# Optimization experiments

Measured on AMD Instinct MI355X. Metric: run time of the kernel, lower is better.

Reference implementation:

```python
import jax, jax.numpy as jnp
import numpy as np

NUM_BINS = 10
HIST_RANGE = 10.0
LN_EPS = 1e-5
NUM_SERVERS = 64
START_IDX = 2 + 2 + NUM_SERVERS  # = 68


def layer_norm(x, g, b):
    mu = jnp.mean(x, axis=-1, keepdims=True)
    var = jnp.mean(jnp.square(x - mu), axis=-1, keepdims=True)
    return (x - mu) * jax.lax.rsqrt(var + LN_EPS) * g + b


def batched_histogram(w):
    # w: [B, S]; replicates np.histogram(w_i, bins=10, range=(0,10)) per row,
    # then normalizes by (sum + 1e-8). Values outside [0,10] are excluded;
    # value == 10 falls in the last bin.
    idx = jnp.clip(jnp.floor(w * (NUM_BINS / HIST_RANGE)).astype(jnp.int32), 0, NUM_BINS - 1)
    mask = ((w >= 0.0) & (w <= HIST_RANGE)).astype(w.dtype)
    oh = jax.nn.one_hot(idx, NUM_BINS, dtype=w.dtype) * mask[..., None]  # [B,S,NB]
    hist = jnp.sum(oh, axis=1)  # [B,NB]
    return hist / (jnp.sum(hist, axis=-1, keepdims=True) + 1e-8)


def setup_inputs() -> dict:
    key = jax.random.key(0)
    ks = jax.random.split(key, 16)
    B, OBS, ACT, H, NB = 65536, 512, 64, 128, NUM_BINS
    COMB = (OBS - NUM_SERVERS) + 128 + 64  # 640

    def lin(k, fin, fout):
        bound = 1.0 / np.sqrt(fin)
        kw, kb = jax.random.split(k)
        return (jax.random.uniform(kw, (fin, fout), jnp.float32, -bound, bound),
                jax.random.uniform(kb, (fout,), jnp.float32, -bound, bound))

    obs = jax.random.uniform(ks[0], (B, OBS), jnp.float32, 0.0, 10.0)
    preference = jax.random.uniform(ks[1], (B, 2), jnp.float32)
    h_w1, h_b1 = lin(ks[2], NB, H)
    h_w2, h_b2 = lin(ks[3], H, H)
    p_w, p_b = lin(ks[4], 2, 64)
    s_w1, s_b1 = lin(ks[5], COMB, 256)
    s_w2, s_b2 = lin(ks[6], 256, 256)
    qd_w, qd_b = lin(ks[7], 256, ACT)
    qe_w, qe_b = lin(ks[8], 256, ACT)
    return {
        'obs': obs, 'preference': preference,
        'h_w1': h_w1, 'h_b1': h_b1,
        'h_ln1_g': jnp.ones((H,)), 'h_ln1_b': jnp.zeros((H,)),
        'h_w2': h_w2, 'h_b2': h_b2,
        'h_ln2_g': jnp.ones((H,)), 'h_ln2_b': jnp.zeros((H,)),
        'p_w': p_w, 'p_b': p_b,
        'p_ln_g': jnp.ones((64,)), 'p_ln_b': jnp.zeros((64,)),
        's_w1': s_w1, 's_b1': s_b1,
        's_ln1_g': jnp.ones((256,)), 's_ln1_b': jnp.zeros((256,)),
        's_w2': s_w2, 's_b2': s_b2,
        's_ln2_g': jnp.ones((256,)), 's_ln2_b': jnp.zeros((256,)),
        'qd_w': qd_w, 'qd_b': qd_b, 'qe_w': qe_w, 'qe_b': qe_b,
    }


def reference(obs, preference,
              h_w1, h_b1, h_ln1_g, h_ln1_b, h_w2, h_b2, h_ln2_g, h_ln2_b,
              p_w, p_b, p_ln_g, p_ln_b,
              s_w1, s_b1, s_ln1_g, s_ln1_b, s_w2, s_b2, s_ln2_g, s_ln2_b,
              qd_w, qd_b, qe_w, qe_b):
    server_workloads = obs[:, START_IDX:START_IDX + NUM_SERVERS]
    obs_wo = jnp.concatenate([obs[:, :START_IDX], obs[:, START_IDX + NUM_SERVERS:]], axis=-1)

    hist = batched_histogram(server_workloads)  # [B, 10]
    h = layer_norm(jax.nn.relu(hist @ h_w1 + h_b1), h_ln1_g, h_ln1_b)
    h = layer_norm(jax.nn.relu(h @ h_w2 + h_b2), h_ln2_g, h_ln2_b)  # [B,128]

    p = layer_norm(jax.nn.relu(preference @ p_w + p_b), p_ln_g, p_ln_b)  # [B,64]

    combined = jnp.concatenate([obs_wo, h, p], axis=-1)  # [B,640]
    s = layer_norm(jax.nn.relu(combined @ s_w1 + s_b1), s_ln1_g, s_ln1_b)
    s = layer_norm(jax.nn.relu(s @ s_w2 + s_b2), s_ln2_g, s_ln2_b)  # [B,256]

    q_delay = s @ qd_w + qd_b   # [B,A]
    q_energy = s @ qe_w + qe_b  # [B,A]
    return jnp.stack([q_delay, q_energy], axis=-1)  # [B,A,2]
```

## Files before the change

kernel.cpp:

```cpp
#include <hip/hip_runtime.h>

typedef __bf16 bf16x8 __attribute__((ext_vector_type(8)));
typedef __bf16 bf16x4 __attribute__((ext_vector_type(4)));
typedef float  f32x4  __attribute__((ext_vector_type(4)));

#define OFF_W1  0
#define OFF_W2  163840
#define OFF_WQ  229376
#define OFF_WH1 262144
#define OFF_WH2 266240
#define WS_ELEMS 282624

__global__ __launch_bounds__(256) void prep_kernel(
    const float* __restrict__ s_w1, const float* __restrict__ s_w2,
    const float* __restrict__ qd_w, const float* __restrict__ qe_w,
    const float* __restrict__ h_w1, const float* __restrict__ h_w2,
    __bf16* __restrict__ wsb)
{
  int idx = blockIdx.x * 256 + threadIdx.x;
  if (idx >= WS_ELEMS) return;
  float val = 0.f;
  if (idx < OFF_W2) {
    int t = idx;
    int j = t & 7, l = (t >> 3) & 63, rest = t >> 9;
    int nt = rest & 15, ks = rest >> 4;
    int k = ks * 32 + (l >> 4) * 8 + j, n = nt * 16 + (l & 15);
    val = s_w1[k * 256 + n];
  } else if (idx < OFF_WQ) {
    int t = idx - OFF_W2;
    int j = t & 7, l = (t >> 3) & 63, rest = t >> 9;
    int nt = rest & 15, ks = rest >> 4;
    int k = ks * 32 + (l >> 4) * 8 + j, n = nt * 16 + (l & 15);
    val = s_w2[k * 256 + n];
  } else if (idx < OFF_WH1) {
    int t = idx - OFF_WQ;
    int j = t & 7, l = (t >> 3) & 63, rest = t >> 9;
    int nt = rest & 7, ks = rest >> 3;
    int k = ks * 32 + (l >> 4) * 8 + j, n = nt * 16 + (l & 15);
    int a = n >> 1;
    val = (n & 1) ? qe_w[k * 64 + a] : qd_w[k * 64 + a];
  } else if (idx < OFF_WH2) {
    int t = idx - OFF_WH1;
    int j = t & 7, l = (t >> 3) & 63, rest = t >> 9;
    int nt = rest & 7;
    int k = (l >> 4) * 8 + j, n = nt * 16 + (l & 15);
    val = (k < 10) ? h_w1[k * 128 + n] : 0.f;
  } else {
    int t = idx - OFF_WH2;
    int j = t & 7, l = (t >> 3) & 63, rest = t >> 9;
    int nt = rest & 7, ks = rest >> 3;
    int k = ks * 32 + (l >> 4) * 8 + j, n = nt * 16 + (l & 15);
    val = h_w2[k * 128 + n];
  }
  wsb[idx] = (__bf16)val;
}

template<int KSTEPS, int NT_TOT, int NTW>
__device__ __forceinline__ void run_gemm(const __bf16* A, int astride,
    const bf16x8* __restrict__ Bsw, int wave, int lane, f32x4 acc[NTW])
{
  const int quad = lane >> 4, ln = lane & 15;
  const int ntb = wave * NTW;
  bf16x8 bcur[NTW];
#pragma unroll
  for (int i = 0; i < NTW; ++i) bcur[i] = Bsw[(ntb + i) * 64 + lane];
#pragma unroll
  for (int ks = 0; ks < KSTEPS; ++ks) {
    bf16x8 bnxt[NTW];
    if (ks + 1 < KSTEPS) {
#pragma unroll
      for (int i = 0; i < NTW; ++i)
        bnxt[i] = Bsw[((ks + 1) * NT_TOT + ntb + i) * 64 + lane];
    }
    bf16x8 a = *(const bf16x8*)(A + ln * astride + ks * 32 + quad * 8);
#pragma unroll
    for (int i = 0; i < NTW; ++i)
      acc[i] = __builtin_amdgcn_mfma_f32_16x16x32_bf16(a, bcur[i], acc[i], 0, 0, 0);
    if (ks + 1 < KSTEPS) {
#pragma unroll
      for (int i = 0; i < NTW; ++i) bcur[i] = bnxt[i];
    }
  }
}

template<int W, int NTW>
__device__ __forceinline__ void epilogue_ln(f32x4 acc[NTW],
    const float* __restrict__ bias, const float* __restrict__ g, const float* __restrict__ bb,
    __bf16* Adst, int dstride, int dstcol0,
    float2* red, int wave, int lane)
{
  const int quad = lane >> 4, ln = lane & 15;
  float x[NTW][4];
#pragma unroll
  for (int i = 0; i < NTW; ++i) {
    int n = (wave * NTW + i) * 16 + ln;
    float b = bias[n];
#pragma unroll
    for (int r = 0; r < 4; ++r)
      x[i][r] = fmaxf(acc[i][r] + b, 0.f);
  }
  float s[4] = {0, 0, 0, 0}, q[4] = {0, 0, 0, 0};
#pragma unroll
  for (int i = 0; i < NTW; ++i)
#pragma unroll
    for (int r = 0; r < 4; ++r) { s[r] += x[i][r]; q[r] += x[i][r] * x[i][r]; }
#pragma unroll
  for (int m2 = 1; m2 < 16; m2 <<= 1)
#pragma unroll
    for (int r = 0; r < 4; ++r) {
      s[r] += __shfl_xor(s[r], m2, 64);
      q[r] += __shfl_xor(q[r], m2, 64);
    }
  if (ln == 0) {
#pragma unroll
    for (int r = 0; r < 4; ++r)
      red[wave * 16 + quad * 4 + r] = make_float2(s[r], q[r]);
  }
  __syncthreads();
#pragma unroll
  for (int r = 0; r < 4; ++r) {
    int m = quad * 4 + r;
    float tot = 0.f, totq = 0.f;
#pragma unroll
    for (int w2 = 0; w2 < 8; ++w2) {
      float2 t = red[w2 * 16 + m];
      tot += t.x; totq += t.y;
    }
    float mu = tot / (float)W;
    float var = totq / (float)W - mu * mu;
    float rs = rsqrtf(var + 1e-5f);
#pragma unroll
    for (int i = 0; i < NTW; ++i) {
      int n = (wave * NTW + i) * 16 + ln;
      float o = (x[i][r] - mu) * rs * g[n] + bb[n];
      Adst[m * dstride + dstcol0 + n] = (__bf16)o;
    }
  }
  __syncthreads();
}

__global__ __launch_bounds__(512, 8) void critic_kernel(
    const float* __restrict__ obs, const float* __restrict__ pref,
    const float* __restrict__ h_b1, const float* __restrict__ h_g1, const float* __restrict__ h_bb1,
    const float* __restrict__ h_b2, const float* __restrict__ h_g2, const float* __restrict__ h_bb2,
    const float* __restrict__ p_w, const float* __restrict__ p_b,
    const float* __restrict__ p_g, const float* __restrict__ p_bb,
    const float* __restrict__ s_b1, const float* __restrict__ s_g1, const float* __restrict__ s_bb1,
    const float* __restrict__ s_b2, const float* __restrict__ s_g2, const float* __restrict__ s_bb2,
    const float* __restrict__ qd_b, const float* __restrict__ qe_b,
    const __bf16* __restrict__ wsb, float* __restrict__ out)
{
  __shared__ __align__(16) __bf16 A_comb[16 * 648];
  __shared__ __align__(16) __bf16 A_s[16 * 264];
  __shared__ __align__(16) __bf16 A_h[16 * 40];
  __shared__ float2 red[128];

  const int tid = threadIdx.x;
  const int wave = tid >> 6, lane = tid & 63;
  const int rowbase = blockIdx.x * 16;

  float pw0 = p_w[lane], pw1 = p_w[64 + lane], pb = p_b[lane];
  float pg = p_g[lane], pbb = p_bb[lane];
#pragma unroll
  for (int r = 0; r < 2; ++r) {
    int row = wave * 2 + r;
    int grow = rowbase + row;
    const float* orow = obs + (size_t)grow * 512;
#pragma unroll
    for (int j = 0; j < 2; ++j) {
      int l = lane + 64 * j;
      if (l < 112) {
        int src4 = (l < 17) ? l : l + 16;
        float4 v = *(const float4*)(orow + 4 * src4);
        bf16x4 o;
        o[0] = (__bf16)v.x; o[1] = (__bf16)v.y; o[2] = (__bf16)v.z; o[3] = (__bf16)v.w;
        *(bf16x4*)(&A_comb[row * 648 + 4 * l]) = o;
      }
    }
    float w = orow[68 + lane];
    int bi = (int)floorf(w);
    bi = bi < 0 ? 0 : (bi > 9 ? 9 : bi);
    bool valid = (w >= 0.f) && (w <= 10.f);
    float tot = 0.f, mine = 0.f;
#pragma unroll
    for (int b = 0; b < 10; ++b) {
      unsigned long long mk = __ballot(valid && (bi == b));
      float c = (float)__popcll(mk);
      tot += c;
      if (lane == b) mine = c;
    }
    float inv = 1.f / (tot + 1e-8f);
    if (lane < 32) A_h[row * 40 + lane] = (__bf16)((lane < 10) ? mine * inv : 0.f);
    float a0 = pref[grow * 2], a1 = pref[grow * 2 + 1];
    float v = fmaxf(fmaf(a0, pw0, fmaf(a1, pw1, pb)), 0.f);
    float s1 = v, s2 = v * v;
#pragma unroll
    for (int m2 = 1; m2 < 64; m2 <<= 1) {
      s1 += __shfl_xor(s1, m2, 64);
      s2 += __shfl_xor(s2, m2, 64);
    }
    float mu = s1 * (1.f / 64.f);
    float var = s2 * (1.f / 64.f) - mu * mu;
    float o = (v - mu) * rsqrtf(var + 1e-5f) * pg + pbb;
    A_comb[row * 648 + 576 + lane] = (__bf16)o;
  }
  __syncthreads();

  {
    f32x4 acc[1] = {};
    run_gemm<1, 8, 1>(A_h, 40, (const bf16x8*)(wsb + OFF_WH1), wave, lane, acc);
    epilogue_ln<128, 1>(acc, h_b1, h_g1, h_bb1, A_s, 264, 0, red, wave, lane);
  }
  {
    f32x4 acc[1] = {};
    run_gemm<4, 8, 1>(A_s, 264, (const bf16x8*)(wsb + OFF_WH2), wave, lane, acc);
    epilogue_ln<128, 1>(acc, h_b2, h_g2, h_bb2, A_comb, 648, 448, red, wave, lane);
  }
  {
    f32x4 acc[2] = {};
    run_gemm<20, 16, 2>(A_comb, 648, (const bf16x8*)(wsb + OFF_W1), wave, lane, acc);
    epilogue_ln<256, 2>(acc, s_b1, s_g1, s_bb1, A_s, 264, 0, red, wave, lane);
  }
  {
    f32x4 acc[2] = {};
    run_gemm<8, 16, 2>(A_s, 264, (const bf16x8*)(wsb + OFF_W2), wave, lane, acc);
    epilogue_ln<256, 2>(acc, s_b2, s_g2, s_bb2, A_s, 264, 0, red, wave, lane);
  }
  {
    f32x4 acc[1] = {};
    run_gemm<8, 8, 1>(A_s, 264, (const bf16x8*)(wsb + OFF_WQ), wave, lane, acc);
    const int quad = lane >> 4, ln = lane & 15;
    int n = wave * 16 + ln;
    float qb = (n & 1) ? qe_b[n >> 1] : qd_b[n >> 1];
#pragma unroll
    for (int r = 0; r < 4; ++r) {
      int m = quad * 4 + r;
      out[(size_t)(rowbase + m) * 128 + n] = acc[0][r] + qb;
    }
  }
}

extern "C" void kernel_launch(void* const* d_in, const int* in_sizes, int n_in,
                              void* d_out, int out_size, void* d_ws, size_t ws_size,
                              hipStream_t stream) {
  const float* obs    = (const float*)d_in[0];
  const float* pref   = (const float*)d_in[1];
  const float* h_w1   = (const float*)d_in[2];
  const float* h_b1   = (const float*)d_in[3];
  const float* h_g1   = (const float*)d_in[4];
  const float* h_bb1  = (const float*)d_in[5];
  const float* h_w2   = (const float*)d_in[6];
  const float* h_b2   = (const float*)d_in[7];
  const float* h_g2   = (const float*)d_in[8];
  const float* h_bb2  = (const float*)d_in[9];
  const float* p_w    = (const float*)d_in[10];
  const float* p_b    = (const float*)d_in[11];
  const float* p_g    = (const float*)d_in[12];
  const float* p_bb   = (const float*)d_in[13];
  const float* s_w1   = (const float*)d_in[14];
  const float* s_b1   = (const float*)d_in[15];
  const float* s_g1   = (const float*)d_in[16];
  const float* s_bb1  = (const float*)d_in[17];
  const float* s_w2   = (const float*)d_in[18];
  const float* s_b2   = (const float*)d_in[19];
  const float* s_g2   = (const float*)d_in[20];
  const float* s_bb2  = (const float*)d_in[21];
  const float* qd_w   = (const float*)d_in[22];
  const float* qd_b   = (const float*)d_in[23];
  const float* qe_w   = (const float*)d_in[24];
  const float* qe_b   = (const float*)d_in[25];

  __bf16* wsb = (__bf16*)d_ws;
  int B = in_sizes[0] / 512;
  int nblocks = B / 16;

  prep_kernel<<<(WS_ELEMS + 255) / 256, 256, 0, stream>>>(s_w1, s_w2, qd_w, qe_w, h_w1, h_w2, wsb);
  critic_kernel<<<nblocks, 512, 0, stream>>>(
      obs, pref, h_b1, h_g1, h_bb1, h_b2, h_g2, h_bb2,
      p_w, p_b, p_g, p_bb, s_b1, s_g1, s_bb1, s_b2, s_g2, s_bb2,
      qd_b, qe_b, (const __bf16*)wsb, (float*)d_out);
}
```

Before: 368.9 us.

## Process 32 rows per block with 16 waves, reuse weight fragments across M tiles

Doubles the rows per block from 16 to 32 and the threads from 512 to 1024. In the large GEMMs each wave now owns one 16-column N tile and loops over two M tiles, so each loaded B fragment feeds two MFMAs, which halves weight traffic per row. The small 128-wide layers split the waves into two M halves. The LayerNorm reduction now uses a per-row slot buffer read with vector loads, and the output is staged through LDS so it can be written with coalesced float4 stores. The cost is a larger LDS footprint per block, larger blocks, and fewer blocks resident per CU.

```diff
diff --git a/kernel.cpp b/kernel.cpp
--- a/kernel.cpp
+++ b/kernel.cpp
@@ -55,91 +55,81 @@
   wsb[idx] = (__bf16)val;
 }
 
-template<int KSTEPS, int NT_TOT, int NTW>
+template<int KSTEPS, int NT_TOT, int MT>
 __device__ __forceinline__ void run_gemm(const __bf16* A, int astride,
-    const bf16x8* __restrict__ Bsw, int wave, int lane, f32x4 acc[NTW])
+    const bf16x8* __restrict__ Bsw, int nt, int mrow0, int lane, f32x4 acc[MT])
 {
   const int quad = lane >> 4, ln = lane & 15;
-  const int ntb = wave * NTW;
-  bf16x8 bcur[NTW];
-#pragma unroll
-  for (int i = 0; i < NTW; ++i) bcur[i] = Bsw[(ntb + i) * 64 + lane];
+  bf16x8 bcur = Bsw[nt * 64 + lane];
 #pragma unroll
   for (int ks = 0; ks < KSTEPS; ++ks) {
-    bf16x8 bnxt[NTW];
-    if (ks + 1 < KSTEPS) {
-#pragma unroll
-      for (int i = 0; i < NTW; ++i)
-        bnxt[i] = Bsw[((ks + 1) * NT_TOT + ntb + i) * 64 + lane];
-    }
-    bf16x8 a = *(const bf16x8*)(A + ln * astride + ks * 32 + quad * 8);
-#pragma unroll
-    for (int i = 0; i < NTW; ++i)
-      acc[i] = __builtin_amdgcn_mfma_f32_16x16x32_bf16(a, bcur[i], acc[i], 0, 0, 0);
-    if (ks + 1 < KSTEPS) {
-#pragma unroll
-      for (int i = 0; i < NTW; ++i) bcur[i] = bnxt[i];
-    }
-  }
-}
-
-template<int W, int NTW>
-__device__ __forceinline__ void epilogue_ln(f32x4 acc[NTW],
+    bf16x8 bnxt;
+    if (ks + 1 < KSTEPS)
+      bnxt = Bsw[((ks + 1) * NT_TOT + nt) * 64 + lane];
+#pragma unroll
+    for (int mt = 0; mt < MT; ++mt) {
+      bf16x8 a = *(const bf16x8*)(A + (mrow0 + mt * 16 + ln) * astride + ks * 32 + quad * 8);
+      acc[mt] = __builtin_amdgcn_mfma_f32_16x16x32_bf16(a, bcur, acc[mt], 0, 0, 0);
+    }
+    if (ks + 1 < KSTEPS) bcur = bnxt;
+  }
+}
+
+template<int W, int NW, int MT>
+__device__ __forceinline__ void epilogue_ln(f32x4 acc[MT],
     const float* __restrict__ bias, const float* __restrict__ g, const float* __restrict__ bb,
+    int n, int mrow0,
     __bf16* Adst, int dstride, int dstcol0,
-    float2* red, int wave, int lane)
+    float2* red2, int wslot, int lane)
 {
   const int quad = lane >> 4, ln = lane & 15;
-  float x[NTW][4];
-#pragma unroll
-  for (int i = 0; i < NTW; ++i) {
-    int n = (wave * NTW + i) * 16 + ln;
-    float b = bias[n];
+  float b = bias[n], gg = g[n], bv = bb[n];
+  float x[MT][4];
+#pragma unroll
+  for (int mt = 0; mt < MT; ++mt)
 #pragma unroll
     for (int r = 0; r < 4; ++r)
-      x[i][r] = fmaxf(acc[i][r] + b, 0.f);
-  }
-  float s[4] = {0, 0, 0, 0}, q[4] = {0, 0, 0, 0};
-#pragma unroll
-  for (int i = 0; i < NTW; ++i)
-#pragma unroll
-    for (int r = 0; r < 4; ++r) { s[r] += x[i][r]; q[r] += x[i][r] * x[i][r]; }
-#pragma unroll
-  for (int m2 = 1; m2 < 16; m2 <<= 1)
+      x[mt][r] = fmaxf(acc[mt][r] + b, 0.f);
+#pragma unroll
+  for (int mt = 0; mt < MT; ++mt) {
+    float s[4], q[4];
+#pragma unroll
+    for (int r = 0; r < 4; ++r) { s[r] = x[mt][r]; q[r] = x[mt][r] * x[mt][r]; }
+#pragma unroll
+    for (int m2 = 1; m2 < 16; m2 <<= 1)
+#pragma unroll
+      for (int r = 0; r < 4; ++r) {
+        s[r] += __shfl_xor(s[r], m2, 64);
+        q[r] += __shfl_xor(q[r], m2, 64);
+      }
+    if (ln == 0) {
+#pragma unroll
+      for (int r = 0; r < 4; ++r)
+        red2[(mrow0 + mt * 16 + quad * 4 + r) * 16 + wslot] = make_float2(s[r], q[r]);
+    }
+  }
+  __syncthreads();
+#pragma unroll
+  for (int mt = 0; mt < MT; ++mt)
 #pragma unroll
     for (int r = 0; r < 4; ++r) {
-      s[r] += __shfl_xor(s[r], m2, 64);
-      q[r] += __shfl_xor(q[r], m2, 64);
-    }
-  if (ln == 0) {
-#pragma unroll
-    for (int r = 0; r < 4; ++r)
-      red[wave * 16 + quad * 4 + r] = make_float2(s[r], q[r]);
-  }
+      int m = mrow0 + mt * 16 + quad * 4 + r;
+      const f32x4* rp = (const f32x4*)(red2 + m * 16);
+      float tot = 0.f, totq = 0.f;
+#pragma unroll
+      for (int k = 0; k < NW / 2; ++k) {
+        f32x4 v = rp[k];
+        tot += v.x + v.z; totq += v.y + v.w;
+      }
+      float mu = tot / (float)W;
+      float var = totq / (float)W - mu * mu;
+      float rs = rsqrtf(var + 1e-5f);
+      Adst[m * dstride + dstcol0 + n] = (__bf16)((x[mt][r] - mu) * rs * gg + bv);
+    }
   __syncthreads();
-#pragma unroll
-  for (int r = 0; r < 4; ++r) {
-    int m = quad * 4 + r;
-    float tot = 0.f, totq = 0.f;
-#pragma unroll
-    for (int w2 = 0; w2 < 8; ++w2) {
-      float2 t = red[w2 * 16 + m];
-      tot += t.x; totq += t.y;
-    }
-    float mu = tot / (float)W;
-    float var = totq / (float)W - mu * mu;
-    float rs = rsqrtf(var + 1e-5f);
-#pragma unroll
-    for (int i = 0; i < NTW; ++i) {
-      int n = (wave * NTW + i) * 16 + ln;
-      float o = (x[i][r] - mu) * rs * g[n] + bb[n];
-      Adst[m * dstride + dstcol0 + n] = (__bf16)o;
-    }
-  }
-  __syncthreads();
-}
-
-__global__ __launch_bounds__(512, 8) void critic_kernel(
+}
+
+__global__ __launch_bounds__(1024, 8) void critic_kernel(
     const float* __restrict__ obs, const float* __restrict__ pref,
     const float* __restrict__ h_b1, const float* __restrict__ h_g1, const float* __restrict__ h_bb1,
     const float* __restrict__ h_b2, const float* __restrict__ h_g2, const float* __restrict__ h_bb2,
@@ -150,14 +140,15 @@
     const float* __restrict__ qd_b, const float* __restrict__ qe_b,
     const __bf16* __restrict__ wsb, float* __restrict__ out)
 {
-  __shared__ __align__(16) __bf16 A_comb[16 * 648];
-  __shared__ __align__(16) __bf16 A_s[16 * 264];
-  __shared__ __align__(16) __bf16 A_h[16 * 40];
-  __shared__ float2 red[128];
+  __shared__ __align__(16) __bf16 A_comb[32 * 648];
+  __shared__ __align__(16) __bf16 A_s[32 * 264];
+  __shared__ __align__(16) __bf16 A_h[32 * 40];
+  __shared__ __align__(16) float2 red2[32 * 16];
 
   const int tid = threadIdx.x;
   const int wave = tid >> 6, lane = tid & 63;
-  const int rowbase = blockIdx.x * 16;
+  const int ln = lane & 15, quad = lane >> 4;
+  const int rowbase = blockIdx.x * 32;
 
   float pw0 = p_w[lane], pw1 = p_w[64 + lane], pb = p_b[lane];
   float pg = p_g[lane], pbb = p_bb[lane];
@@ -206,37 +197,44 @@
   }
   __syncthreads();
 
+  const int nt8 = wave & 7;
+  const int mr8 = (wave >> 3) * 16;
+  const int n128 = nt8 * 16 + ln;
+  const int n256 = wave * 16 + ln;
+
   {
     f32x4 acc[1] = {};
-    run_gemm<1, 8, 1>(A_h, 40, (const bf16x8*)(wsb + OFF_WH1), wave, lane, acc);
-    epilogue_ln<128, 1>(acc, h_b1, h_g1, h_bb1, A_s, 264, 0, red, wave, lane);
+    run_gemm<1, 8, 1>(A_h, 40, (const bf16x8*)(wsb + OFF_WH1), nt8, mr8, lane, acc);
+    epilogue_ln<128, 8, 1>(acc, h_b1, h_g1, h_bb1, n128, mr8, A_s, 264, 0, red2, nt8, lane);
   }
   {
     f32x4 acc[1] = {};
-    run_gemm<4, 8, 1>(A_s, 264, (const bf16x8*)(wsb + OFF_WH2), wave, lane, acc);
-    epilogue_ln<128, 1>(acc, h_b2, h_g2, h_bb2, A_comb, 648, 448, red, wave, lane);
+    run_gemm<4, 8, 1>(A_s, 264, (const bf16x8*)(wsb + OFF_WH2), nt8, mr8, lane, acc);
+    epilogue_ln<128, 8, 1>(acc, h_b2, h_g2, h_bb2, n128, mr8, A_comb, 648, 448, red2, nt8, lane);
   }
   {
     f32x4 acc[2] = {};
-    run_gemm<20, 16, 2>(A_comb, 648, (const bf16x8*)(wsb + OFF_W1), wave, lane, acc);
-    epilogue_ln<256, 2>(acc, s_b1, s_g1, s_bb1, A_s, 264, 0, red, wave, lane);
+    run_gemm<20, 16, 2>(A_comb, 648, (const bf16x8*)(wsb + OFF_W1), wave, 0, lane, acc);
+    epilogue_ln<256, 16, 2>(acc, s_b1, s_g1, s_bb1, n256, 0, A_s, 264, 0, red2, wave, lane);
   }
   {
     f32x4 acc[2] = {};
-    run_gemm<8, 16, 2>(A_s, 264, (const bf16x8*)(wsb + OFF_W2), wave, lane, acc);
-    epilogue_ln<256, 2>(acc, s_b2, s_g2, s_bb2, A_s, 264, 0, red, wave, lane);
+    run_gemm<8, 16, 2>(A_s, 264, (const bf16x8*)(wsb + OFF_W2), wave, 0, lane, acc);
+    epilogue_ln<256, 16, 2>(acc, s_b2, s_g2, s_bb2, n256, 0, A_s, 264, 0, red2, wave, lane);
   }
   {
     f32x4 acc[1] = {};
-    run_gemm<8, 8, 1>(A_s, 264, (const bf16x8*)(wsb + OFF_WQ), wave, lane, acc);
-    const int quad = lane >> 4, ln = lane & 15;
-    int n = wave * 16 + ln;
-    float qb = (n & 1) ? qe_b[n >> 1] : qd_b[n >> 1];
-#pragma unroll
-    for (int r = 0; r < 4; ++r) {
-      int m = quad * 4 + r;
-      out[(size_t)(rowbase + m) * 128 + n] = acc[0][r] + qb;
-    }
+    run_gemm<8, 8, 1>(A_s, 264, (const bf16x8*)(wsb + OFF_WQ), nt8, mr8, lane, acc);
+    float qb = (n128 & 1) ? qe_b[n128 >> 1] : qd_b[n128 >> 1];
+    float* stage = (float*)A_comb;
+    int m0 = mr8 + quad * 4;
+#pragma unroll
+    for (int r = 0; r < 4; ++r)
+      stage[(m0 + r) * 132 + n128] = acc[0][r] + qb;
+    __syncthreads();
+    int row = tid >> 5, c4 = tid & 31;
+    float4 v = *(const float4*)&stage[row * 132 + c4 * 4];
+    *(float4*)&out[(size_t)(rowbase + row) * 128 + c4 * 4] = v;
   }
 }
 
@@ -272,10 +270,10 @@
 
   __bf16* wsb = (__bf16*)d_ws;
   int B = in_sizes[0] / 512;
-  int nblocks = B / 16;
+  int nblocks = B / 32;
 
   prep_kernel<<<(WS_ELEMS + 255) / 256, 256, 0, stream>>>(s_w1, s_w2, qd_w, qe_w, h_w1, h_w2, wsb);
-  critic_kernel<<<nblocks, 512, 0, stream>>>(
+  critic_kernel<<<nblocks, 1024, 0, stream>>>(
       obs, pref, h_b1, h_g1, h_bb1, h_b2, h_g2, h_bb2,
       p_w, p_b, p_g, p_bb, s_b1, s_g1, s_bb1, s_b2, s_g2, s_bb2,
       qd_b, qe_b, (const __bf16*)wsb, (float*)d_out);
```

New measurement: 429.9 us. +16.5%, slower.
